# Optimization experiments

Measured on AMD Instinct MI355X. Metric: run time of the kernel, lower is better.

Reference implementation:

```python
import jax, jax.numpy as jnp
import numpy as np

N_NODES = 100000
N_EDGES = 1200000
N_GRAPHS = 128
D = 64  # input_size == num_classes == 64


def setup_inputs() -> dict:
    key = jax.random.key(0)
    ks = jax.random.split(key, 8)
    feats = jax.random.normal(ks[0], (N_NODES, D), dtype=jnp.float32)
    src = jax.random.randint(ks[1], (N_EDGES,), 0, N_NODES, dtype=jnp.int64)
    dst = jax.random.randint(ks[2], (N_EDGES,), 0, N_NODES, dtype=jnp.int64)
    graph_id = jnp.sort(jax.random.randint(ks[3], (N_NODES,), 0, N_GRAPHS, dtype=jnp.int64))
    # Linear layer params (torch nn.Linear: y = x @ W.T + b); store as [in, out]
    s = 1.0 / np.sqrt(D)
    W1 = jax.random.uniform(ks[4], (D, D), jnp.float32, -s, s)
    b1 = jax.random.uniform(ks[5], (D,), jnp.float32, -s, s)
    W2 = jax.random.uniform(ks[6], (D, D), jnp.float32, -s, s)
    b2 = jax.random.uniform(ks[7], (D,), jnp.float32, -s, s)
    return {"feats": feats, "src": src, "dst": dst, "graph_id": graph_id,
            "W1": W1, "b1": b1, "W2": W2, "b2": b2}


def reference(feats, src, dst, graph_id, W1, b1, W2, b2):
    # GINConv (sum aggregator, eps=0): h = Linear(x + sum_{j in N(i)} x_j)
    agg1 = jax.ops.segment_sum(feats[src], dst, num_segments=N_NODES)
    h = jax.nn.relu((feats + agg1) @ W1 + b1)
    agg2 = jax.ops.segment_sum(h[src], dst, num_segments=N_NODES)
    h2 = (h + agg2) @ W2 + b2
    # SumPooling: per-graph sum of node features -> [N_GRAPHS, D]
    return jax.ops.segment_sum(h2, graph_id, num_segments=N_GRAPHS)
```

## Files before the change

### kernel.cpp

```cpp
#include <hip/hip_runtime.h>

#define D 64
#define NNODES 100000
#define NGRAPHS 128
#define NTILES ((NNODES + 15) / 16)
#define BUCKW 512
#define NBUCK ((NNODES + BUCKW - 1) / BUCKW)
#define EPB 4096

typedef unsigned int uint;
typedef unsigned short ushort;
typedef __attribute__((ext_vector_type(8))) short short8;
typedef __attribute__((ext_vector_type(4))) float f32x4;

__device__ __forceinline__ ushort f2b(float f) {
    uint u = __float_as_uint(f);
    uint r = (u + 0x7fffu + ((u >> 16) & 1u)) >> 16;
    return (ushort)r;
}
__device__ __forceinline__ float b2f(ushort h) {
    return __uint_as_float(((uint)h) << 16);
}

__global__ void zero_kernel(int* __restrict__ buf, int n4) {
    int i = blockIdx.x * blockDim.x + threadIdx.x;
    int stride = gridDim.x * blockDim.x;
    int4 z = make_int4(0, 0, 0, 0);
    for (; i < n4; i += stride) ((int4*)buf)[i] = z;
}

__global__ void cast_kernel(const float* __restrict__ in, ushort* __restrict__ outb, int n4) {
    int i = blockIdx.x * blockDim.x + threadIdx.x;
    int stride = gridDim.x * blockDim.x;
    for (; i < n4; i += stride) {
        float4 v = ((const float4*)in)[i];
        ushort4 o;
        o.x = f2b(v.x); o.y = f2b(v.y); o.z = f2b(v.z); o.w = f2b(v.w);
        ((ushort4*)outb)[i] = o;
    }
}

__global__ void prep_w_kernel(const float* __restrict__ W, ushort* __restrict__ Wswz) {
    int t = threadIdx.x;
    int j = t >> 6, lane = t & 63;
    int c = j >> 1, h = j & 1;
    int col = 16 * c + (lane & 15);
    int kbase = (lane >> 4) * 8 + 32 * h;
#pragma unroll
    for (int i = 0; i < 8; ++i)
        Wswz[(size_t)t * 8 + i] = f2b(W[(kbase + i) * D + col]);
}

__global__ void bhist_kernel(const int* __restrict__ dst, int* __restrict__ ghist,
                             int nE, int nblk) {
    __shared__ int lh[NBUCK];
    int t = threadIdx.x, blk = blockIdx.x;
    for (int i = t; i < NBUCK; i += 256) lh[i] = 0;
    __syncthreads();
    int base = blk * EPB + t * 16;
    if (base + 16 <= nE) {
#pragma unroll
        for (int j = 0; j < 4; ++j) {
            int4 d = *(const int4*)(dst + base + j * 4);
            atomicAdd(&lh[d.x >> 9], 1);
            atomicAdd(&lh[d.y >> 9], 1);
            atomicAdd(&lh[d.z >> 9], 1);
            atomicAdd(&lh[d.w >> 9], 1);
        }
    } else {
        int lim = min(base + 16, nE);
        for (int e = base; e < lim; ++e) atomicAdd(&lh[dst[e] >> 9], 1);
    }
    __syncthreads();
    for (int i = t; i < NBUCK; i += 256) ghist[(size_t)i * nblk + blk] = lh[i];
}

__global__ void gpartial_kernel(const int* __restrict__ g, int* __restrict__ gsum, int M) {
    __shared__ int sh[256];
    int t = threadIdx.x;
    int base = (blockIdx.x * 256 + t) * 4;
    int s = 0;
    if (base + 4 <= M) {
        int4 v = *(const int4*)(g + base);
        s = v.x + v.y + v.z + v.w;
    } else {
        for (int i = base; i < M; ++i) s += g[i];
    }
    sh[t] = s;
    __syncthreads();
    for (int d = 128; d > 0; d >>= 1) {
        if (t < d) sh[t] += sh[t + d];
        __syncthreads();
    }
    if (t == 0) gsum[blockIdx.x] = sh[0];
}

__global__ void gscanb_kernel(const int* __restrict__ gsum, int* __restrict__ gbase2,
                              int* __restrict__ bbase, int* __restrict__ off,
                              int nb, int nE) {
    __shared__ int sh[256];
    int t = threadIdx.x;
    sh[t] = (t < nb) ? gsum[t] : 0;
    __syncthreads();
    for (int d = 1; d < 256; d <<= 1) {
        int u = (t >= d) ? sh[t - d] : 0;
        __syncthreads();
        sh[t] += u;
        __syncthreads();
    }
    if (t < nb) gbase2[t] = (t == 0) ? 0 : sh[t - 1];
    if (t == 0) {
        bbase[NBUCK] = nE;
        off[NNODES] = nE;
    }
}

__global__ void goffsets_kernel(int* __restrict__ g, const int* __restrict__ gbase2,
                                int* __restrict__ bbase, int M, int nblk) {
    __shared__ int sh[256];
    int t = threadIdx.x;
    int base = (blockIdx.x * 256 + t) * 4;
    int v0 = 0, v1 = 0, v2 = 0, v3 = 0;
    if (base + 4 <= M) {
        int4 v = *(const int4*)(g + base);
        v0 = v.x; v1 = v.y; v2 = v.z; v3 = v.w;
    } else {
        if (base < M)     v0 = g[base];
        if (base + 1 < M) v1 = g[base + 1];
        if (base + 2 < M) v2 = g[base + 2];
        if (base + 3 < M) v3 = g[base + 3];
    }
    int s = v0 + v1 + v2 + v3;
    sh[t] = s;
    __syncthreads();
    for (int d = 1; d < 256; d <<= 1) {
        int u = (t >= d) ? sh[t - d] : 0;
        __syncthreads();
        sh[t] += u;
        __syncthreads();
    }
    int e0 = gbase2[blockIdx.x] + sh[t] - s;
    int e1 = e0 + v0, e2 = e1 + v1, e3 = e2 + v2;
    if (base + 4 <= M) {
        *(int4*)(g + base) = make_int4(e0, e1, e2, e3);
    } else {
        if (base < M)     g[base]     = e0;
        if (base + 1 < M) g[base + 1] = e1;
        if (base + 2 < M) g[base + 2] = e2;
        if (base + 3 < M) g[base + 3] = e3;
    }
    int ev[4] = {e0, e1, e2, e3};
#pragma unroll
    for (int j = 0; j < 4; ++j) {
        int i = base + j;
        if (i < M && i % nblk == 0) bbase[i / nblk] = ev[j];
    }
}

__global__ void bscatter_kernel(const int* __restrict__ src, const int* __restrict__ dst,
                                const int* __restrict__ gbase, int* __restrict__ packed,
                                int nE, int nblk) {
    __shared__ int lcur[NBUCK];
    int t = threadIdx.x, blk = blockIdx.x;
    for (int i = t; i < NBUCK; i += 256) lcur[i] = gbase[(size_t)i * nblk + blk];
    __syncthreads();
    int base = blk * EPB + t * 16;
    if (base + 16 <= nE) {
#pragma unroll
        for (int j = 0; j < 4; ++j) {
            int4 d = *(const int4*)(dst + base + j * 4);
            int4 s4 = *(const int4*)(src + base + j * 4);
            int p0 = atomicAdd(&lcur[d.x >> 9], 1);
            int p1 = atomicAdd(&lcur[d.y >> 9], 1);
            int p2 = atomicAdd(&lcur[d.z >> 9], 1);
            int p3 = atomicAdd(&lcur[d.w >> 9], 1);
            packed[p0] = (s4.x << 9) | (d.x & 511);
            packed[p1] = (s4.y << 9) | (d.y & 511);
            packed[p2] = (s4.z << 9) | (d.z & 511);
            packed[p3] = (s4.w << 9) | (d.w & 511);
        }
    } else {
        int lim = min(base + 16, nE);
        for (int e = base; e < lim; ++e) {
            int p = atomicAdd(&lcur[dst[e] >> 9], 1);
            packed[p] = (src[e] << 9) | (dst[e] & 511);
        }
    }
}

__global__ void csr_build_kernel(const int* __restrict__ packed, const int* __restrict__ bbase,
                                 const int* __restrict__ gid,
                                 int* __restrict__ off, int* __restrict__ esrc,
                                 int* __restrict__ egid) {
    __shared__ int lcnt[BUCKW];
    __shared__ int lcur[BUCKW];
    __shared__ int lgid[BUCKW];
    __shared__ int part[256];
    int t = threadIdx.x;
    int blk = blockIdx.x;
    int ebeg = bbase[blk], eend = bbase[blk + 1];
    lcnt[t] = 0; lcnt[t + 256] = 0;
    int n0 = blk * BUCKW + t, n1 = blk * BUCKW + t + 256;
    lgid[t]       = (n0 < NNODES) ? gid[n0] : 0;
    lgid[t + 256] = (n1 < NNODES) ? gid[n1] : 0;
    __syncthreads();
    for (int e = ebeg + t; e < eend; e += 256)
        atomicAdd(&lcnt[packed[e] & 511], 1);
    __syncthreads();
    int a = lcnt[2 * t], bv = lcnt[2 * t + 1];
    part[t] = a + bv;
    __syncthreads();
    for (int d = 1; d < 256; d <<= 1) {
        int u = (t >= d) ? part[t - d] : 0;
        __syncthreads();
        part[t] += u;
        __syncthreads();
    }
    int excl2 = (t == 0) ? 0 : part[t - 1];
    lcur[2 * t] = excl2;
    lcur[2 * t + 1] = excl2 + a;
    int node0 = blk * BUCKW + 2 * t;
    if (node0 < NNODES)     off[node0]     = ebeg + excl2;
    if (node0 + 1 < NNODES) off[node0 + 1] = ebeg + excl2 + a;
    __syncthreads();
    for (int e = ebeg + t; e < eend; e += 256) {
        int p = packed[e];
        int loc = p & 511;
        int pos = ebeg + atomicAdd(&lcur[loc], 1);
        esrc[pos] = p >> 9;
        egid[pos] = lgid[loc];
    }
}

__global__ void gather_gemm1_kernel(const ushort* __restrict__ xb,
                                    const int* __restrict__ off,
                                    const int* __restrict__ esrc,
                                    const ushort* __restrict__ Wswz,
                                    const float* __restrict__ b1,
                                    ushort* __restrict__ hb, int ntiles) {
    int tid = threadIdx.x;
    int w = tid >> 6, lane = tid & 63;
    int tile = blockIdx.x * 4 + w;
    if (tile >= ntiles) return;

    short8 bfrag[8];
#pragma unroll
    for (int j = 0; j < 8; ++j)
        bfrag[j] = *(const short8*)(Wswz + ((size_t)j * 64 + lane) * 8);

    int r = lane & 15, h = lane >> 4;
    int rbase = tile * 16;
    int node = rbase + r;

    float accA[8], accB[8];
    {
        const ushort* p = xb + (size_t)node * D + h * 8;
        short8 sA = *(const short8*)(p);
        short8 sB = *(const short8*)(p + 32);
#pragma unroll
        for (int q = 0; q < 8; ++q) {
            accA[q] = b2f((ushort)sA[q]);
            accB[q] = b2f((ushort)sB[q]);
        }
    }

    int beg = off[node], end = off[node + 1];
    int i = beg;
    for (; i + 4 <= end; i += 4) {
        int e0 = esrc[i], e1 = esrc[i + 1], e2 = esrc[i + 2], e3 = esrc[i + 3];
        const ushort* p0 = xb + (size_t)e0 * D + h * 8;
        const ushort* p1 = xb + (size_t)e1 * D + h * 8;
        const ushort* p2 = xb + (size_t)e2 * D + h * 8;
        const ushort* p3 = xb + (size_t)e3 * D + h * 8;
        short8 v0A = *(const short8*)(p0), v0B = *(const short8*)(p0 + 32);
        short8 v1A = *(const short8*)(p1), v1B = *(const short8*)(p1 + 32);
        short8 v2A = *(const short8*)(p2), v2B = *(const short8*)(p2 + 32);
        short8 v3A = *(const short8*)(p3), v3B = *(const short8*)(p3 + 32);
#pragma unroll
        for (int q = 0; q < 8; ++q) {
            accA[q] += (b2f((ushort)v0A[q]) + b2f((ushort)v1A[q]))
                     + (b2f((ushort)v2A[q]) + b2f((ushort)v3A[q]));
            accB[q] += (b2f((ushort)v0B[q]) + b2f((ushort)v1B[q]))
                     + (b2f((ushort)v2B[q]) + b2f((ushort)v3B[q]));
        }
    }
    for (; i < end; ++i) {
        const ushort* p = xb + (size_t)esrc[i] * D + h * 8;
        short8 vA = *(const short8*)(p), vB = *(const short8*)(p + 32);
#pragma unroll
        for (int q = 0; q < 8; ++q) {
            accA[q] += b2f((ushort)vA[q]);
            accB[q] += b2f((ushort)vB[q]);
        }
    }

    short8 a0, a1;
#pragma unroll
    for (int q = 0; q < 8; ++q) {
        a0[q] = (short)f2b(accA[q]);
        a1[q] = (short)f2b(accB[q]);
    }

    f32x4 acc0 = {0.f, 0.f, 0.f, 0.f};
    f32x4 acc1 = {0.f, 0.f, 0.f, 0.f};
    f32x4 acc2 = {0.f, 0.f, 0.f, 0.f};
    f32x4 acc3 = {0.f, 0.f, 0.f, 0.f};
    acc0 = __builtin_amdgcn_mfma_f32_16x16x32_bf16(a0, bfrag[0], acc0, 0, 0, 0);
    acc0 = __builtin_amdgcn_mfma_f32_16x16x32_bf16(a1, bfrag[1], acc0, 0, 0, 0);
    acc1 = __builtin_amdgcn_mfma_f32_16x16x32_bf16(a0, bfrag[2], acc1, 0, 0, 0);
    acc1 = __builtin_amdgcn_mfma_f32_16x16x32_bf16(a1, bfrag[3], acc1, 0, 0, 0);
    acc2 = __builtin_amdgcn_mfma_f32_16x16x32_bf16(a0, bfrag[4], acc2, 0, 0, 0);
    acc2 = __builtin_amdgcn_mfma_f32_16x16x32_bf16(a1, bfrag[5], acc2, 0, 0, 0);
    acc3 = __builtin_amdgcn_mfma_f32_16x16x32_bf16(a0, bfrag[6], acc3, 0, 0, 0);
    acc3 = __builtin_amdgcn_mfma_f32_16x16x32_bf16(a1, bfrag[7], acc3, 0, 0, 0);

    int colb = lane & 15;
    int rowb = (lane >> 4) * 4;
#pragma unroll
    for (int rr = 0; rr < 4; ++rr) {
        size_t rowoff = (size_t)(rbase + rowb + rr) * D;
        hb[rowoff + colb +  0] = f2b(fmaxf(acc0[rr] + b1[colb +  0], 0.f));
        hb[rowoff + colb + 16] = f2b(fmaxf(acc1[rr] + b1[colb + 16], 0.f));
        hb[rowoff + colb + 32] = f2b(fmaxf(acc2[rr] + b1[colb + 32], 0.f));
        hb[rowoff + colb + 48] = f2b(fmaxf(acc3[rr] + b1[colb + 48], 0.f));
    }
}

__global__ void pool_self_kernel(const ushort* __restrict__ hb,
                                 const int* __restrict__ gid,
                                 float* __restrict__ P,
                                 float* __restrict__ cntg, int n) {
    int tid = threadIdx.x;
    int w = tid >> 6, lane = tid & 63;
    int waves_total = gridDim.x * 4;
    int wave_id = blockIdx.x * 4 + w;
    int chunk = (n + waves_total - 1) / waves_total;
    int start = wave_id * chunk;
    int end = min(start + chunk, n);

    float accp = 0.f;
    int cur = -1, cc = 0;
    for (int node = start; node < end; ++node) {
        float v = b2f(hb[(size_t)node * D + lane]);
        int g = gid[node];
        if (g != cur) {
            if (cur >= 0) {
                atomicAdd(&P[cur * D + lane], accp);
                if (lane == 0) atomicAdd(&cntg[cur], (float)cc);
            }
            cur = g; accp = 0.f; cc = 0;
        }
        accp += v;
        cc++;
    }
    if (cur >= 0) {
        atomicAdd(&P[cur * D + lane], accp);
        if (lane == 0) atomicAdd(&cntg[cur], (float)cc);
    }
}

__global__ void edge_pool_kernel(const ushort* __restrict__ hb,
                                 const int* __restrict__ esrc,
                                 const int* __restrict__ egid,
                                 float* __restrict__ P, int nE) {
    int tid = threadIdx.x;
    int w = tid >> 6, lane = tid & 63;
    int waves_total = gridDim.x * 4;
    int wave_id = blockIdx.x * 4 + w;
    int chunk = ((nE + waves_total - 1) / waves_total + 15) & ~15;
    int start = wave_id * chunk;
    int end = min(start + chunk, nE);
    if (start >= nE) return;

    float accp = 0.f;
    int cur = -1;
    int i = start;
    for (; i + 16 <= end; i += 16) {
        int4 s0 = *(const int4*)(esrc + i);
        int4 s1 = *(const int4*)(esrc + i + 4);
        int4 s2 = *(const int4*)(esrc + i + 8);
        int4 s3 = *(const int4*)(esrc + i + 12);
        int4 g0 = *(const int4*)(egid + i);
        int4 g1 = *(const int4*)(egid + i + 4);
        int4 g2 = *(const int4*)(egid + i + 8);
        int4 g3 = *(const int4*)(egid + i + 12);
        ushort v0  = hb[(size_t)s0.x * D + lane];
        ushort v1  = hb[(size_t)s0.y * D + lane];
        ushort v2  = hb[(size_t)s0.z * D + lane];
        ushort v3  = hb[(size_t)s0.w * D + lane];
        ushort v4  = hb[(size_t)s1.x * D + lane];
        ushort v5  = hb[(size_t)s1.y * D + lane];
        ushort v6  = hb[(size_t)s1.z * D + lane];
        ushort v7  = hb[(size_t)s1.w * D + lane];
        ushort v8  = hb[(size_t)s2.x * D + lane];
        ushort v9  = hb[(size_t)s2.y * D + lane];
        ushort v10 = hb[(size_t)s2.z * D + lane];
        ushort v11 = hb[(size_t)s2.w * D + lane];
        ushort v12 = hb[(size_t)s3.x * D + lane];
        ushort v13 = hb[(size_t)s3.y * D + lane];
        ushort v14 = hb[(size_t)s3.z * D + lane];
        ushort v15 = hb[(size_t)s3.w * D + lane];
        int gg[16] = {g0.x, g0.y, g0.z, g0.w, g1.x, g1.y, g1.z, g1.w,
                      g2.x, g2.y, g2.z, g2.w, g3.x, g3.y, g3.z, g3.w};
        ushort vv[16] = {v0, v1, v2, v3, v4, v5, v6, v7,
                         v8, v9, v10, v11, v12, v13, v14, v15};
        if (gg[0] == cur && gg[15] == cur) {
            float s = ((b2f(vv[0]) + b2f(vv[1])) + (b2f(vv[2]) + b2f(vv[3])))
                    + ((b2f(vv[4]) + b2f(vv[5])) + (b2f(vv[6]) + b2f(vv[7])))
                    + ((b2f(vv[8]) + b2f(vv[9])) + (b2f(vv[10]) + b2f(vv[11])))
                    + ((b2f(vv[12]) + b2f(vv[13])) + (b2f(vv[14]) + b2f(vv[15])));
            accp += s;
        } else {
#pragma unroll
            for (int q = 0; q < 16; ++q) {
                if (gg[q] != cur) {
                    if (cur >= 0) atomicAdd(&P[cur * D + lane], accp);
                    cur = gg[q]; accp = 0.f;
                }
                accp += b2f(vv[q]);
            }
        }
    }
    for (; i < end; ++i) {
        int g = egid[i];
        ushort v = hb[(size_t)esrc[i] * D + lane];
        if (g != cur) {
            if (cur >= 0) atomicAdd(&P[cur * D + lane], accp);
            cur = g; accp = 0.f;
        }
        accp += b2f(v);
    }
    if (cur >= 0) atomicAdd(&P[cur * D + lane], accp);
}

__global__ void final_kernel(const float* __restrict__ P,
                             const float* __restrict__ cntg,
                             const float* __restrict__ W2,
                             const float* __restrict__ b2,
                             float* __restrict__ out) {
    __shared__ float Ws[D * D];
    __shared__ float bs[D];
    __shared__ float xs[4][D];
    int tid = threadIdx.x;
    for (int i = tid; i < D * D / 4; i += blockDim.x)
        ((float4*)Ws)[i] = ((const float4*)W2)[i];
    if (tid < D) bs[tid] = b2[tid];
    __syncthreads();

    int w = tid >> 6, lane = tid & 63;
    int g = blockIdx.x * 4 + w;
    if (g >= NGRAPHS) return;
    xs[w][lane] = P[g * D + lane];
    float acc = cntg[g] * bs[lane];
#pragma unroll
    for (int k = 0; k < D; ++k)
        acc = fmaf(xs[w][k], Ws[k * D + lane], acc);
    out[g * D + lane] = acc;
}

extern "C" void kernel_launch(void* const* d_in, const int* in_sizes, int n_in,
                              void* d_out, int out_size, void* d_ws, size_t ws_size,
                              hipStream_t stream) {
    const float* feats = (const float*)d_in[0];
    const int*   src   = (const int*)d_in[1];
    const int*   dst   = (const int*)d_in[2];
    const int*   gid   = (const int*)d_in[3];
    const float* W1    = (const float*)d_in[4];
    const float* b1    = (const float*)d_in[5];
    const float* W2    = (const float*)d_in[6];
    const float* b2    = (const float*)d_in[7];
    float* out = (float*)d_out;

    int nE = in_sizes[1];
    int nblk = (nE + EPB - 1) / EPB;
    int M = NBUCK * nblk;
    int gb = (M + 1023) / 1024;

    int*    bbase  = (int*)d_ws;
    int*    gsum   = bbase + 256;
    int*    gbase2 = gsum + 256;
    float*  P      = (float*)(gbase2 + 256);
    float*  cntg   = P + NGRAPHS * D;
    int*    off    = (int*)(cntg + 128);
    int*    ghist  = off + ((NNODES + 7) & ~3);
    int*    packed = ghist + ((M + 3) & ~3);
    int*    esrc   = packed + ((nE + 3) & ~3);
    int*    egid   = esrc + ((nE + 3) & ~3);
    ushort* Wswz   = (ushort*)(egid + ((nE + 3) & ~3));
    ushort* xb     = Wswz + 4096;
    ushort* hb     = xb + (size_t)NNODES * D;

    bhist_kernel<<<nblk, 256, 0, stream>>>(dst, ghist, nE, nblk);
    gpartial_kernel<<<gb, 256, 0, stream>>>(ghist, gsum, M);
    gscanb_kernel<<<1, 256, 0, stream>>>(gsum, gbase2, bbase, off, gb, nE);
    goffsets_kernel<<<gb, 256, 0, stream>>>(ghist, gbase2, bbase, M, nblk);
    bscatter_kernel<<<nblk, 256, 0, stream>>>(src, dst, ghist, packed, nE, nblk);
    csr_build_kernel<<<NBUCK, 256, 0, stream>>>(packed, bbase, gid, off, esrc, egid);

    cast_kernel<<<2048, 256, 0, stream>>>(feats, xb, NNODES * D / 4);
    prep_w_kernel<<<1, 512, 0, stream>>>(W1, Wswz);
    zero_kernel<<<8, 256, 0, stream>>>((int*)P, (NGRAPHS * D + 128) / 4);

    gather_gemm1_kernel<<<(NTILES + 3) / 4, 256, 0, stream>>>(xb, off, esrc, Wswz, b1, hb, NTILES);

    pool_self_kernel<<<512, 256, 0, stream>>>(hb, gid, P, cntg, NNODES);
    edge_pool_kernel<<<2048, 256, 0, stream>>>(hb, esrc, egid, P, nE);
    final_kernel<<<NGRAPHS / 4, 256, 0, stream>>>(P, cntg, W2, b2, out);
}
```

Before: 164.8 us.

## Fuse prep kernels and pooling kernels into fewer launches; widen CSR build blocks

Merges the dst histogram, feature bf16 cast, W1 swizzle and P zeroing into one block-partitioned kernel, and merges the self-pool and edge-pool kernels into one launch. The CSR build kernel now runs with 512 threads per block, one thread per node. The aim is to remove launch gaps and let independent work share the GPU concurrently. The cost is heterogeneous blocks in one grid and a longer scan loop in the CSR build.

```diff
diff --git a/kernel.cpp b/kernel.cpp
--- a/kernel.cpp
+++ b/kernel.cpp
@@ -7,6 +7,9 @@
 #define BUCKW 512
 #define NBUCK ((NNODES + BUCKW - 1) / BUCKW)
 #define EPB 4096
+#define CASTB 1600
+#define SELFB 512
+#define EDGEB 2048
 
 typedef unsigned int uint;
 typedef unsigned short ushort;
@@ -22,57 +25,57 @@
     return __uint_as_float(((uint)h) << 16);
 }
 
-__global__ void zero_kernel(int* __restrict__ buf, int n4) {
-    int i = blockIdx.x * blockDim.x + threadIdx.x;
-    int stride = gridDim.x * blockDim.x;
-    int4 z = make_int4(0, 0, 0, 0);
-    for (; i < n4; i += stride) ((int4*)buf)[i] = z;
-}
-
-__global__ void cast_kernel(const float* __restrict__ in, ushort* __restrict__ outb, int n4) {
-    int i = blockIdx.x * blockDim.x + threadIdx.x;
-    int stride = gridDim.x * blockDim.x;
-    for (; i < n4; i += stride) {
-        float4 v = ((const float4*)in)[i];
-        ushort4 o;
-        o.x = f2b(v.x); o.y = f2b(v.y); o.z = f2b(v.z); o.w = f2b(v.w);
-        ((ushort4*)outb)[i] = o;
-    }
-}
-
-__global__ void prep_w_kernel(const float* __restrict__ W, ushort* __restrict__ Wswz) {
-    int t = threadIdx.x;
-    int j = t >> 6, lane = t & 63;
-    int c = j >> 1, h = j & 1;
-    int col = 16 * c + (lane & 15);
-    int kbase = (lane >> 4) * 8 + 32 * h;
-#pragma unroll
-    for (int i = 0; i < 8; ++i)
-        Wswz[(size_t)t * 8 + i] = f2b(W[(kbase + i) * D + col]);
-}
-
-__global__ void bhist_kernel(const int* __restrict__ dst, int* __restrict__ ghist,
-                             int nE, int nblk) {
+__global__ void prep_fused_kernel(const float* __restrict__ feats, ushort* __restrict__ xb,
+                                  const int* __restrict__ dst, int* __restrict__ ghist,
+                                  const float* __restrict__ W1, ushort* __restrict__ Wswz,
+                                  float* __restrict__ P, int nE, int nblk) {
     __shared__ int lh[NBUCK];
     int t = threadIdx.x, blk = blockIdx.x;
-    for (int i = t; i < NBUCK; i += 256) lh[i] = 0;
-    __syncthreads();
-    int base = blk * EPB + t * 16;
-    if (base + 16 <= nE) {
-#pragma unroll
-        for (int j = 0; j < 4; ++j) {
-            int4 d = *(const int4*)(dst + base + j * 4);
-            atomicAdd(&lh[d.x >> 9], 1);
-            atomicAdd(&lh[d.y >> 9], 1);
-            atomicAdd(&lh[d.z >> 9], 1);
-            atomicAdd(&lh[d.w >> 9], 1);
+    if (blk < nblk) {
+        for (int i = t; i < NBUCK; i += 256) lh[i] = 0;
+        __syncthreads();
+        int base = blk * EPB + t * 16;
+        if (base + 16 <= nE) {
+#pragma unroll
+            for (int j = 0; j < 4; ++j) {
+                int4 d = *(const int4*)(dst + base + j * 4);
+                atomicAdd(&lh[d.x >> 9], 1);
+                atomicAdd(&lh[d.y >> 9], 1);
+                atomicAdd(&lh[d.z >> 9], 1);
+                atomicAdd(&lh[d.w >> 9], 1);
+            }
+        } else {
+            int lim = min(base + 16, nE);
+            for (int e = base; e < lim; ++e) atomicAdd(&lh[dst[e] >> 9], 1);
+        }
+        __syncthreads();
+        for (int i = t; i < NBUCK; i += 256) ghist[(size_t)i * nblk + blk] = lh[i];
+    } else if (blk < nblk + CASTB) {
+        int i = (blk - nblk) * 256 + t;
+        int stride = CASTB * 256;
+        int n4 = NNODES * D / 4;
+        for (; i < n4; i += stride) {
+            float4 v = ((const float4*)feats)[i];
+            ushort4 o;
+            o.x = f2b(v.x); o.y = f2b(v.y); o.z = f2b(v.z); o.w = f2b(v.w);
+            ((ushort4*)xb)[i] = o;
+        }
+    } else if (blk == nblk + CASTB) {
+        for (int half = 0; half < 2; ++half) {
+            int tt = t + half * 256;
+            int j = tt >> 6, lane = tt & 63;
+            int c = j >> 1, h = j & 1;
+            int col = 16 * c + (lane & 15);
+            int kbase = (lane >> 4) * 8 + 32 * h;
+#pragma unroll
+            for (int i = 0; i < 8; ++i)
+                Wswz[(size_t)tt * 8 + i] = f2b(W1[(kbase + i) * D + col]);
         }
     } else {
-        int lim = min(base + 16, nE);
-        for (int e = base; e < lim; ++e) atomicAdd(&lh[dst[e] >> 9], 1);
-    }
-    __syncthreads();
-    for (int i = t; i < NBUCK; i += 256) ghist[(size_t)i * nblk + blk] = lh[i];
+        int n4 = (NGRAPHS * D + 128) / 4;
+        for (int i = t; i < n4; i += 256)
+            ((int4*)P)[i] = make_int4(0, 0, 0, 0);
+    }
 }
 
 __global__ void gpartial_kernel(const int* __restrict__ g, int* __restrict__ gsum, int M) {
@@ -195,35 +198,31 @@
     __shared__ int lcnt[BUCKW];
     __shared__ int lcur[BUCKW];
     __shared__ int lgid[BUCKW];
-    __shared__ int part[256];
+    __shared__ int part[BUCKW];
     int t = threadIdx.x;
     int blk = blockIdx.x;
     int ebeg = bbase[blk], eend = bbase[blk + 1];
-    lcnt[t] = 0; lcnt[t + 256] = 0;
-    int n0 = blk * BUCKW + t, n1 = blk * BUCKW + t + 256;
-    lgid[t]       = (n0 < NNODES) ? gid[n0] : 0;
-    lgid[t + 256] = (n1 < NNODES) ? gid[n1] : 0;
-    __syncthreads();
-    for (int e = ebeg + t; e < eend; e += 256)
+    lcnt[t] = 0;
+    int n0 = blk * BUCKW + t;
+    lgid[t] = (n0 < NNODES) ? gid[n0] : 0;
+    __syncthreads();
+    for (int e = ebeg + t; e < eend; e += 512)
         atomicAdd(&lcnt[packed[e] & 511], 1);
     __syncthreads();
-    int a = lcnt[2 * t], bv = lcnt[2 * t + 1];
-    part[t] = a + bv;
-    __syncthreads();
-    for (int d = 1; d < 256; d <<= 1) {
+    int v = lcnt[t];
+    part[t] = v;
+    __syncthreads();
+    for (int d = 1; d < 512; d <<= 1) {
         int u = (t >= d) ? part[t - d] : 0;
         __syncthreads();
         part[t] += u;
         __syncthreads();
     }
-    int excl2 = (t == 0) ? 0 : part[t - 1];
-    lcur[2 * t] = excl2;
-    lcur[2 * t + 1] = excl2 + a;
-    int node0 = blk * BUCKW + 2 * t;
-    if (node0 < NNODES)     off[node0]     = ebeg + excl2;
-    if (node0 + 1 < NNODES) off[node0 + 1] = ebeg + excl2 + a;
-    __syncthreads();
-    for (int e = ebeg + t; e < eend; e += 256) {
+    int excl = part[t] - v;
+    lcur[t] = excl;
+    if (n0 < NNODES) off[n0] = ebeg + excl;
+    __syncthreads();
+    for (int e = ebeg + t; e < eend; e += 512) {
         int p = packed[e];
         int loc = p & 511;
         int pos = ebeg + atomicAdd(&lcur[loc], 1);
@@ -326,47 +325,46 @@
     }
 }
 
-__global__ void pool_self_kernel(const ushort* __restrict__ hb,
-                                 const int* __restrict__ gid,
-                                 float* __restrict__ P,
-                                 float* __restrict__ cntg, int n) {
+__global__ void pool_fused_kernel(const ushort* __restrict__ hb,
+                                  const int* __restrict__ gid,
+                                  const int* __restrict__ esrc,
+                                  const int* __restrict__ egid,
+                                  float* __restrict__ P,
+                                  float* __restrict__ cntg, int n, int nE) {
     int tid = threadIdx.x;
     int w = tid >> 6, lane = tid & 63;
-    int waves_total = gridDim.x * 4;
-    int wave_id = blockIdx.x * 4 + w;
-    int chunk = (n + waves_total - 1) / waves_total;
-    int start = wave_id * chunk;
-    int end = min(start + chunk, n);
-
-    float accp = 0.f;
-    int cur = -1, cc = 0;
-    for (int node = start; node < end; ++node) {
-        float v = b2f(hb[(size_t)node * D + lane]);
-        int g = gid[node];
-        if (g != cur) {
-            if (cur >= 0) {
-                atomicAdd(&P[cur * D + lane], accp);
-                if (lane == 0) atomicAdd(&cntg[cur], (float)cc);
+    int blk = blockIdx.x;
+
+    if (blk < SELFB) {
+        int waves_total = SELFB * 4;
+        int wave_id = blk * 4 + w;
+        int chunk = (n + waves_total - 1) / waves_total;
+        int start = wave_id * chunk;
+        int end = min(start + chunk, n);
+        float accp = 0.f;
+        int cur = -1, cc = 0;
+        for (int node = start; node < end; ++node) {
+            float v = b2f(hb[(size_t)node * D + lane]);
+            int g = gid[node];
+            if (g != cur) {
+                if (cur >= 0) {
+                    atomicAdd(&P[cur * D + lane], accp);
+                    if (lane == 0) atomicAdd(&cntg[cur], (float)cc);
+                }
+                cur = g; accp = 0.f; cc = 0;
             }
-            cur = g; accp = 0.f; cc = 0;
-        }
-        accp += v;
-        cc++;
-    }
-    if (cur >= 0) {
-        atomicAdd(&P[cur * D + lane], accp);
-        if (lane == 0) atomicAdd(&cntg[cur], (float)cc);
-    }
-}
-
-__global__ void edge_pool_kernel(const ushort* __restrict__ hb,
-                                 const int* __restrict__ esrc,
-                                 const int* __restrict__ egid,
-                                 float* __restrict__ P, int nE) {
-    int tid = threadIdx.x;
-    int w = tid >> 6, lane = tid & 63;
-    int waves_total = gridDim.x * 4;
-    int wave_id = blockIdx.x * 4 + w;
+            accp += v;
+            cc++;
+        }
+        if (cur >= 0) {
+            atomicAdd(&P[cur * D + lane], accp);
+            if (lane == 0) atomicAdd(&cntg[cur], (float)cc);
+        }
+        return;
+    }
+
+    int waves_total = EDGEB * 4;
+    int wave_id = (blk - SELFB) * 4 + w;
     int chunk = ((nE + waves_total - 1) / waves_total + 15) & ~15;
     int start = wave_id * chunk;
     int end = min(start + chunk, nE);
@@ -490,20 +488,19 @@
     ushort* xb     = Wswz + 4096;
     ushort* hb     = xb + (size_t)NNODES * D;
 
-    bhist_kernel<<<nblk, 256, 0, stream>>>(dst, ghist, nE, nblk);
+    prep_fused_kernel<<<nblk + CASTB + 2, 256, 0, stream>>>(
+        feats, xb, dst, ghist, W1, Wswz, P, nE, nblk);
+
     gpartial_kernel<<<gb, 256, 0, stream>>>(ghist, gsum, M);
     gscanb_kernel<<<1, 256, 0, stream>>>(gsum, gbase2, bbase, off, gb, nE);
     goffsets_kernel<<<gb, 256, 0, stream>>>(ghist, gbase2, bbase, M, nblk);
+
     bscatter_kernel<<<nblk, 256, 0, stream>>>(src, dst, ghist, packed, nE, nblk);
-    csr_build_kernel<<<NBUCK, 256, 0, stream>>>(packed, bbase, gid, off, esrc, egid);
-
-    cast_kernel<<<2048, 256, 0, stream>>>(feats, xb, NNODES * D / 4);
-    prep_w_kernel<<<1, 512, 0, stream>>>(W1, Wswz);
-    zero_kernel<<<8, 256, 0, stream>>>((int*)P, (NGRAPHS * D + 128) / 4);
+    csr_build_kernel<<<NBUCK, 512, 0, stream>>>(packed, bbase, gid, off, esrc, egid);
 
     gather_gemm1_kernel<<<(NTILES + 3) / 4, 256, 0, stream>>>(xb, off, esrc, Wswz, b1, hb, NTILES);
 
-    pool_self_kernel<<<512, 256, 0, stream>>>(hb, gid, P, cntg, NNODES);
-    edge_pool_kernel<<<2048, 256, 0, stream>>>(hb, esrc, egid, P, nE);
+    pool_fused_kernel<<<SELFB + EDGEB, 256, 0, stream>>>(hb, gid, esrc, egid, P, cntg, NNODES, nE);
+
     final_kernel<<<NGRAPHS / 4, 256, 0, stream>>>(P, cntg, W2, b2, out);
 }
```

Measured after the change: 138.3 us, median of 2. -16.1%, faster.
